# Optimization experiments

Hardware: AMD Instinct MI355X
Metric: run time of the kernel (lower is better)

The kernel has to match this reference:

```python
import jax, jax.numpy as jnp
import numpy as np

K = 3          # kernel_size
PAD = 1        # padding
FOCAL = 50.0
DMIN = 1.0
DMAX = 50.0
ORIG_H = 512.0  # original_image_size[1]


def setup_inputs() -> dict:
    key = jax.random.key(0)
    k1, k2 = jax.random.split(key)
    x = jax.random.normal(k1, (4, 64, 256, 256), dtype=jnp.float32)
    # conv weight [out_ch, in_ch, K, K] (bias=False)
    W = jax.random.normal(k2, (64, 64, K, K), dtype=jnp.float32) * 0.05
    return {"x": x, "W": W}


def _bilinear(img, xs, ys):
    """Bilinear sample img [B,C,H,W] at float pixel coords xs, ys [B,Ho,Wo].
    Zero padding outside the image (grid_sample semantics)."""
    B, C, H, Wd = img.shape
    Ho, Wo = xs.shape[1], xs.shape[2]
    x0 = jnp.floor(xs); y0 = jnp.floor(ys)
    wx1 = xs - x0; wx0 = 1.0 - wx1
    wy1 = ys - y0; wy0 = 1.0 - wy1
    img_flat = img.reshape(B, C, H * Wd)

    def gat(ix, iy):
        ixi = ix.astype(jnp.int32); iyi = iy.astype(jnp.int32)
        valid = (ixi >= 0) & (ixi < Wd) & (iyi >= 0) & (iyi < H)
        idx = jnp.clip(iyi, 0, H - 1) * Wd + jnp.clip(ixi, 0, Wd - 1)
        v = jnp.take_along_axis(img_flat, idx.reshape(B, 1, Ho * Wo), axis=2)
        v = v.reshape(B, C, Ho, Wo)
        return v * valid[:, None].astype(img.dtype)

    return (gat(x0, y0) * (wx0 * wy0)[:, None]
            + gat(x0 + 1, y0) * (wx1 * wy0)[:, None]
            + gat(x0, y0 + 1) * (wx0 * wy1)[:, None]
            + gat(x0 + 1, y0 + 1) * (wx1 * wy1)[:, None])


def reference(x, W):
    B, C, H, Wd = x.shape
    downsample = ORIG_H / H  # 2.0 for H=256

    # upper branch: plain 3x3 conv, padding 1, no bias
    x_upper = jax.lax.conv_general_dilated(x, W, (1, 1), [(PAD, PAD), (PAD, PAD)])

    # geometry -> clamped depth (geometry_method='max', formulation='depth')
    depth = jnp.clip(jnp.max(x, axis=1), DMIN, DMAX)  # [B,H,W]

    # Frontal homography: Hom01 = I with [1,2] = focal/(downsample*depth);
    # its inverse Hom10 shifts y by -s.
    s = FOCAL / (downsample * depth)  # [B,H,W]

    xi = jnp.arange(Wd, dtype=x.dtype)[None, None, :]
    yi = jnp.arange(H, dtype=x.dtype)[None, :, None]
    xs = jnp.broadcast_to(xi, (B, H, Wd))
    ys = yi - s  # Hom10 applied to pixel coords

    # warp input with per-pixel Hom10 (pass_warped_images=True)
    x2 = _bilinear(x, xs, ys)

    # deformable conv: per-pixel offset from Hom10 is (dx,dy)=(0,-s) for all 9 taps
    x_lower = jnp.zeros_like(x_upper)
    for ky in range(K):
        for kx in range(K):
            sx = xs + (kx - PAD)
            sy = ys + (ky - PAD)
            tap = _bilinear(x2, sx, sy)  # [B,C,H,W]
            x_lower = x_lower + jnp.einsum('bchw,oc->bohw', tap, W[:, :, ky, kx])

    # project with 'min' over the stacked (upper, lower) branches
    return jnp.minimum(x_upper, x_lower)
```

## Files before the change

### kernel.cpp

```cpp
#include <hip/hip_runtime.h>
#include <cmath>

constexpr int BB = 4, CC = 64, HH = 256, WW = 256;
constexpr int WP = 258;
constexpr int C2R = 257;

typedef short short8 __attribute__((ext_vector_type(8)));
typedef float f32x4 __attribute__((ext_vector_type(4)));
#define MFMA_BF16 __builtin_amdgcn_mfma_f32_16x16x32_bf16

union U16x8 { uint4 v; unsigned short h[8]; };

__device__ inline unsigned short f2bf(float f) {
  unsigned u = __builtin_bit_cast(unsigned, f);
  u += 0x7fffu + ((u >> 16) & 1u);
  return (unsigned short)(u >> 16);
}
__device__ inline float bf2f(unsigned short h) {
  unsigned u = ((unsigned)h) << 16;
  return __builtin_bit_cast(float, u);
}

__global__ __launch_bounds__(256, 2) void k_pack(const float* __restrict__ x,
                                                 float* __restrict__ s,
                                                 unsigned short* __restrict__ xn) {
  __shared__ float tile[CC * 257];
  const int t = threadIdx.x, y = blockIdx.x, b = blockIdx.y;
  const float* base = x + (size_t)b * CC * HH * WW + y * WW + t;
  float m = -1e30f;
#pragma unroll 8
  for (int c = 0; c < CC; ++c) {
    float v = base[(size_t)c * HH * WW];
    tile[c * 257 + t] = v;
    m = fmaxf(m, v);
  }
  s[(b * HH + y) * WW + t] = 25.0f / fminf(fmaxf(m, 1.0f), 50.0f);
  uint4* xn4 = (uint4*)xn;
  if (t < 16) {
    int col = (t >> 3) ? (WP - 1) : 0, c8 = t & 7;
    xn4[(((size_t)(b * HH + y) * WP + col) * CC + c8 * 8) >> 3] =
        make_uint4(0, 0, 0, 0);
  }
  __syncthreads();
#pragma unroll
  for (int g = 0; g < 8; ++g) {
    int px = g * 32 + (t >> 3), c8 = t & 7;
    U16x8 r;
#pragma unroll
    for (int j = 0; j < 8; ++j) r.h[j] = f2bf(tile[(c8 * 8 + j) * 257 + px]);
    xn4[(((size_t)(b * HH + y) * WP + px + 1) * CC + c8 * 8) >> 3] = r.v;
  }
}

__global__ __launch_bounds__(256) void k_wpack(const float* __restrict__ Wt,
                                               unsigned short* __restrict__ Wp) {
  int gid = blockIdx.x * 256 + threadIdx.x;
  int lane = gid & 63, kc = (gid >> 6) & 1, mt = (gid >> 7) & 3, tap = gid >> 9;
  int o = mt * 16 + (lane & 15);
  int kb = kc * 32 + (lane >> 4) * 8;
  int ky = tap / 3, kx = tap % 3;
  U16x8 r;
#pragma unroll
  for (int j = 0; j < 8; ++j)
    r.h[j] = f2bf(Wt[o * 576 + (kb + j) * 9 + ky * 3 + kx]);
  ((uint4*)Wp)[gid] = r.v;
}

__global__ __launch_bounds__(256) void k_warp(const unsigned short* __restrict__ xn,
                                              const float* __restrict__ s,
                                              unsigned short* __restrict__ x2) {
  const int t = threadIdx.x, r = blockIdx.x, b = blockIdx.y;
  const uint4* xn4 = (const uint4*)xn;
  uint4* x24 = (uint4*)x2;
  if (t < 16) {
    int col = (t >> 3) ? (WP - 1) : 0, c8 = t & 7;
    x24[(((size_t)(b * HH + r) * WP + col) * CC + c8 * 8) >> 3] =
        make_uint4(0, 0, 0, 0);
  }
#pragma unroll
  for (int g = 0; g < 8; ++g) {
    int px = g * 32 + (t >> 3), c8 = t & 7;
    float sv = s[(b * HH + r) * WW + px];
    float ys = (float)r - sv;
    float fy = floorf(ys);
    float wfr = ys - fy;
    int i0 = (int)fy;
    float w0 = (i0 >= 0 && i0 < HH) ? 1.0f - wfr : 0.0f;
    float w1 = (i0 + 1 >= 0 && i0 + 1 < HH) ? wfr : 0.0f;
    int a0 = min(max(i0, 0), HH - 1), a1 = min(max(i0 + 1, 0), HH - 1);
    U16x8 u0, u1, rr;
    u0.v = xn4[(((size_t)(b * HH + a0) * WP + px + 1) * CC + c8 * 8) >> 3];
    u1.v = xn4[(((size_t)(b * HH + a1) * WP + px + 1) * CC + c8 * 8) >> 3];
#pragma unroll
    for (int k = 0; k < 8; ++k)
      rr.h[k] = f2bf(w0 * bf2f(u0.h[k]) + w1 * bf2f(u1.h[k]));
    x24[(((size_t)(b * HH + r) * WP + px + 1) * CC + c8 * 8) >> 3] = rr.v;
  }
}

#define STAGE_TILE(src4, rowBase, colBase, bb)                                 \
  do {                                                                         \
    for (int i = 0; i < 13; ++i) {                                             \
      int idx = i * 256 + t;                                                   \
      if (idx < 3168) {                                                        \
        int rr_ = idx / 528, rem = idx % 528;                                  \
        int col_ = rem >> 3, ch_ = rem & 7;                                    \
        int xrow = (rowBase) + rr_;                                            \
        uint4 v = make_uint4(0, 0, 0, 0);                                      \
        if (xrow >= 0 && xrow < HH)                                            \
          v = src4[((size_t)((bb)*HH + xrow) * WP + (colBase) + col_) * 8 + ch_]; \
        lds[(rr_ * 66 + col_) * 8 + (ch_ ^ (col_ & 7))] = v;                   \
      }                                                                        \
    }                                                                          \
  } while (0)

__global__ __launch_bounds__(256, 2) void k_lower(const unsigned short* __restrict__ x2,
                                                  const unsigned short* __restrict__ Wp,
                                                  unsigned short* __restrict__ c2) {
  __shared__ uint4 lds[3168];
  const int t = threadIdx.x;
  const int ctile = blockIdx.x & 3, tr = blockIdx.x >> 2;
  const int b = blockIdx.y;
  const int r0 = tr * 4 - 1;
  const int colBase = ctile * 64;

  const uint4* src4 = (const uint4*)x2;
  STAGE_TILE(src4, r0 - 1, colBase, b);

  const int lane = t & 63, w = t >> 6;
  const int ow = w & 1, rg = w >> 1, lr = rg * 2;
  const int quad = lane >> 4, l15 = lane & 15;

  short8 wf[9][2][2];
  const uint4* wp4 = (const uint4*)Wp;
#pragma unroll
  for (int tap = 0; tap < 9; ++tap)
#pragma unroll
    for (int ct = 0; ct < 2; ++ct)
#pragma unroll
      for (int kc = 0; kc < 2; ++kc)
        wf[tap][ct][kc] = __builtin_bit_cast(
            short8, wp4[((tap * 4 + (ow * 2 + ct)) * 2 + kc) * 64 + lane]);
  __syncthreads();

#pragma unroll 1
  for (int pt = 0; pt < 4; ++pt) {
    f32x4 acc[2][2] = {{{0.f, 0.f, 0.f, 0.f}, {0.f, 0.f, 0.f, 0.f}},
                       {{0.f, 0.f, 0.f, 0.f}, {0.f, 0.f, 0.f, 0.f}}};
#pragma unroll
    for (int ir = 0; ir < 4; ++ir) {
      int ldr = lr + ir;
#pragma unroll
      for (int kx = 0; kx < 3; ++kx) {
        int col = pt * 16 + l15 + kx;
        int cb = (ldr * 66 + col) * 8, sw = col & 7;
#pragma unroll
        for (int kc = 0; kc < 2; ++kc) {
          short8 xf = __builtin_bit_cast(short8, lds[cb + ((kc * 4 + quad) ^ sw)]);
          if (ir <= 2) {
#pragma unroll
            for (int ct = 0; ct < 2; ++ct)
              acc[0][ct] = MFMA_BF16(wf[ir * 3 + kx][ct][kc], xf, acc[0][ct], 0, 0, 0);
          }
          if (ir >= 1) {
#pragma unroll
            for (int ct = 0; ct < 2; ++ct)
              acc[1][ct] = MFMA_BF16(wf[(ir - 1) * 3 + kx][ct][kc], xf, acc[1][ct], 0, 0, 0);
          }
        }
      }
    }
#pragma unroll
    for (int rr = 0; rr < 2; ++rr) {
      int r = r0 + lr + rr;
      if (r > 255) continue;
      int px = colBase + pt * 16 + l15;
#pragma unroll
      for (int ct = 0; ct < 2; ++ct) {
        f32x4 A = acc[rr][ct];
        int ch = (ow * 2 + ct) * 16 + quad * 4;
        unsigned short h0 = f2bf(A[0]), h1 = f2bf(A[1]), h2 = f2bf(A[2]), h3 = f2bf(A[3]);
        uint2 val = make_uint2((unsigned)h0 | ((unsigned)h1 << 16),
                               (unsigned)h2 | ((unsigned)h3 << 16));
        *(uint2*)(c2 + (((size_t)(b * C2R + (r + 1)) * WW + px) * CC + ch)) = val;
      }
    }
  }
}

__global__ __launch_bounds__(256, 2) void k_final(const unsigned short* __restrict__ xn,
                                                  const unsigned short* __restrict__ Wp,
                                                  const float* __restrict__ s,
                                                  const unsigned short* __restrict__ c2,
                                                  float* __restrict__ out) {
  __shared__ uint4 lds[3168];
  const int t = threadIdx.x;
  const int ctile = blockIdx.x & 3, tr = blockIdx.x >> 2;
  const int b = blockIdx.y;
  const int y0 = tr * 4;
  const int colBase = ctile * 64;

  const uint4* src4 = (const uint4*)xn;
  STAGE_TILE(src4, y0 - 1, colBase, b);

  const int lane = t & 63, w = t >> 6;
  const int ow = w & 1, rg = w >> 1, lr = rg * 2;
  const int quad = lane >> 4, l15 = lane & 15;

  short8 wf[9][2][2];
  const uint4* wp4 = (const uint4*)Wp;
#pragma unroll
  for (int tap = 0; tap < 9; ++tap)
#pragma unroll
    for (int ct = 0; ct < 2; ++ct)
#pragma unroll
      for (int kc = 0; kc < 2; ++kc)
        wf[tap][ct][kc] = __builtin_bit_cast(
            short8, wp4[((tap * 4 + (ow * 2 + ct)) * 2 + kc) * 64 + lane]);
  __syncthreads();

#pragma unroll 1
  for (int pt = 0; pt < 4; ++pt) {
    f32x4 acc[2][2] = {{{0.f, 0.f, 0.f, 0.f}, {0.f, 0.f, 0.f, 0.f}},
                       {{0.f, 0.f, 0.f, 0.f}, {0.f, 0.f, 0.f, 0.f}}};
#pragma unroll
    for (int ir = 0; ir < 4; ++ir) {
      int ldr = lr + ir;
#pragma unroll
      for (int kx = 0; kx < 3; ++kx) {
        int col = pt * 16 + l15 + kx;
        int cb = (ldr * 66 + col) * 8, sw = col & 7;
#pragma unroll
        for (int kc = 0; kc < 2; ++kc) {
          short8 xf = __builtin_bit_cast(short8, lds[cb + ((kc * 4 + quad) ^ sw)]);
          if (ir <= 2) {
#pragma unroll
            for (int ct = 0; ct < 2; ++ct)
              acc[0][ct] = MFMA_BF16(xf, wf[ir * 3 + kx][ct][kc], acc[0][ct], 0, 0, 0);
          }
          if (ir >= 1) {
#pragma unroll
            for (int ct = 0; ct < 2; ++ct)
              acc[1][ct] = MFMA_BF16(xf, wf[(ir - 1) * 3 + kx][ct][kc], acc[1][ct], 0, 0, 0);
          }
        }
      }
    }
#pragma unroll
    for (int rr = 0; rr < 2; ++rr) {
      int y = y0 + lr + rr;
      int px0 = colBase + pt * 16 + quad * 4;
      f32x4 sv4 = *(const f32x4*)(s + (b * HH + y) * WW + px0);
      float lw0[4], lw1[4];
      int a0i[4], a1i[4];
#pragma unroll
      for (int j = 0; j < 4; ++j) {
        float ys = (float)y - sv4[j];
        float fy = floorf(ys);
        float wfr = ys - fy;
        int i0 = (int)fy;
        lw0[j] = (i0 + 1 >= 0 && i0 + 1 <= HH) ? 1.0f - wfr : 0.0f;
        lw1[j] = (i0 + 2 >= 0 && i0 + 2 <= HH) ? wfr : 0.0f;
        a0i[j] = min(max(i0 + 1, 0), HH);
        a1i[j] = min(max(i0 + 2, 0), HH);
      }
#pragma unroll
      for (int ct = 0; ct < 2; ++ct) {
        f32x4 A = acc[rr][ct];
        int ch = (ow * 2 + ct) * 16 + l15;
        f32x4 res;
#pragma unroll
        for (int j = 0; j < 4; ++j) {
          int px = px0 + j;
          float v0 = bf2f(c2[((size_t)(b * C2R + a0i[j]) * WW + px) * CC + ch]);
          float v1 = bf2f(c2[((size_t)(b * C2R + a1i[j]) * WW + px) * CC + ch]);
          res[j] = fminf(A[j], lw0[j] * v0 + lw1[j] * v1);
        }
        *(f32x4*)(out + ((size_t)(b * CC + ch) * HH + y) * WW + px0) = res;
      }
    }
  }
}

extern "C" void kernel_launch(void* const* d_in, const int* in_sizes, int n_in,
                              void* d_out, int out_size, void* d_ws, size_t ws_size,
                              hipStream_t stream) {
  const float* x = (const float*)d_in[0];
  const float* Wt = (const float*)d_in[1];
  float* out = (float*)d_out;

  char* ws = (char*)d_ws;
  float* s = (float*)ws;
  unsigned short* Wp = (unsigned short*)(ws + 1048576);
  unsigned short* xn = (unsigned short*)(ws + 1122304);
  unsigned short* x2 = (unsigned short*)(ws + 34938880);
  unsigned short* c2 = (unsigned short*)(ws + 68755456);
  k_pack<<<dim3(HH, BB), 256, 0, stream>>>(x, s, xn);
  k_wpack<<<dim3(18), 256, 0, stream>>>(Wt, Wp);
  k_warp<<<dim3(HH, BB), 256, 0, stream>>>(xn, s, x2);
  k_lower<<<dim3(4 * 65, BB), 256, 0, stream>>>(x2, Wp, c2);
  k_final<<<dim3(4 * 64, BB), 256, 0, stream>>>(xn, Wp, s, c2, out);
}
```

Before: 216.6 us.

## Fuse vertical warp into lower-conv tile staging and transpose final MFMA output mapping

Removes the separate k_warp kernel and its x2 intermediate buffer, and recomputes the bilinear vertical warp on the fly while staging the input tile into LDS in k_lower. This cuts one launch and a full write plus read of a bf16 tensor, at the cost of recomputing the warp for halo rows and doing two gathered loads per staged element. The final kernel's MFMA operands are swapped so each lane holds four consecutive channels, which allows vectorized loads from c2 but turns the output stores into scalar strided writes. The fused path also rounds to bf16 by truncation instead of round-to-nearest.

```diff
diff --git a/kernel.cpp b/kernel.cpp
--- a/kernel.cpp
+++ b/kernel.cpp
@@ -10,11 +10,15 @@
 #define MFMA_BF16 __builtin_amdgcn_mfma_f32_16x16x32_bf16
 
 union U16x8 { uint4 v; unsigned short h[8]; };
+union U16x4 { uint2 v; unsigned short h[4]; };
 
 __device__ inline unsigned short f2bf(float f) {
   unsigned u = __builtin_bit_cast(unsigned, f);
   u += 0x7fffu + ((u >> 16) & 1u);
   return (unsigned short)(u >> 16);
+}
+__device__ inline unsigned short f2bf_trunc(float f) {
+  return (unsigned short)(__builtin_bit_cast(unsigned, f) >> 16);
 }
 __device__ inline float bf2f(unsigned short h) {
   unsigned u = ((unsigned)h) << 16;
@@ -64,38 +68,6 @@
   for (int j = 0; j < 8; ++j)
     r.h[j] = f2bf(Wt[o * 576 + (kb + j) * 9 + ky * 3 + kx]);
   ((uint4*)Wp)[gid] = r.v;
-}
-
-__global__ __launch_bounds__(256) void k_warp(const unsigned short* __restrict__ xn,
-                                              const float* __restrict__ s,
-                                              unsigned short* __restrict__ x2) {
-  const int t = threadIdx.x, r = blockIdx.x, b = blockIdx.y;
-  const uint4* xn4 = (const uint4*)xn;
-  uint4* x24 = (uint4*)x2;
-  if (t < 16) {
-    int col = (t >> 3) ? (WP - 1) : 0, c8 = t & 7;
-    x24[(((size_t)(b * HH + r) * WP + col) * CC + c8 * 8) >> 3] =
-        make_uint4(0, 0, 0, 0);
-  }
-#pragma unroll
-  for (int g = 0; g < 8; ++g) {
-    int px = g * 32 + (t >> 3), c8 = t & 7;
-    float sv = s[(b * HH + r) * WW + px];
-    float ys = (float)r - sv;
-    float fy = floorf(ys);
-    float wfr = ys - fy;
-    int i0 = (int)fy;
-    float w0 = (i0 >= 0 && i0 < HH) ? 1.0f - wfr : 0.0f;
-    float w1 = (i0 + 1 >= 0 && i0 + 1 < HH) ? wfr : 0.0f;
-    int a0 = min(max(i0, 0), HH - 1), a1 = min(max(i0 + 1, 0), HH - 1);
-    U16x8 u0, u1, rr;
-    u0.v = xn4[(((size_t)(b * HH + a0) * WP + px + 1) * CC + c8 * 8) >> 3];
-    u1.v = xn4[(((size_t)(b * HH + a1) * WP + px + 1) * CC + c8 * 8) >> 3];
-#pragma unroll
-    for (int k = 0; k < 8; ++k)
-      rr.h[k] = f2bf(w0 * bf2f(u0.h[k]) + w1 * bf2f(u1.h[k]));
-    x24[(((size_t)(b * HH + r) * WP + px + 1) * CC + c8 * 8) >> 3] = rr.v;
-  }
 }
 
 #define STAGE_TILE(src4, rowBase, colBase, bb)                                 \
@@ -114,8 +86,9 @@
     }                                                                          \
   } while (0)
 
-__global__ __launch_bounds__(256, 2) void k_lower(const unsigned short* __restrict__ x2,
+__global__ __launch_bounds__(256, 2) void k_lower(const unsigned short* __restrict__ xn,
                                                   const unsigned short* __restrict__ Wp,
+                                                  const float* __restrict__ s,
                                                   unsigned short* __restrict__ c2) {
   __shared__ uint4 lds[3168];
   const int t = threadIdx.x;
@@ -124,8 +97,36 @@
   const int r0 = tr * 4 - 1;
   const int colBase = ctile * 64;
 
-  const uint4* src4 = (const uint4*)x2;
-  STAGE_TILE(src4, r0 - 1, colBase, b);
+  const uint4* xn4 = (const uint4*)xn;
+  for (int i = 0; i < 13; ++i) {
+    int idx = i * 256 + t;
+    if (idx < 3168) {
+      int rr_ = idx / 528, rem = idx % 528;
+      int col_ = rem >> 3, ch_ = rem & 7;
+      int xrow = r0 - 1 + rr_;
+      uint4 v = make_uint4(0, 0, 0, 0);
+      if (xrow >= 0 && xrow < HH) {
+        int px = colBase + col_ - 1;
+        int pxc = min(max(px, 0), WW - 1);
+        float sv = s[(b * HH + xrow) * WW + pxc];
+        float ys = (float)xrow - sv;
+        float fy = floorf(ys);
+        float wfr = ys - fy;
+        int i0 = (int)fy;
+        float w0 = (i0 >= 0) ? 1.0f - wfr : 0.0f;
+        float w1 = (i0 + 1 >= 0) ? wfr : 0.0f;
+        int a0 = max(i0, 0), a1 = max(i0 + 1, 0);
+        U16x8 u0, u1, rr;
+        u0.v = xn4[((size_t)(b * HH + a0) * WP + colBase + col_) * 8 + ch_];
+        u1.v = xn4[((size_t)(b * HH + a1) * WP + colBase + col_) * 8 + ch_];
+#pragma unroll
+        for (int k = 0; k < 8; ++k)
+          rr.h[k] = f2bf_trunc(w0 * bf2f(u0.h[k]) + w1 * bf2f(u1.h[k]));
+        v = rr.v;
+      }
+      lds[(rr_ * 66 + col_) * 8 + (ch_ ^ (col_ & 7))] = v;
+    }
+  }
 
   const int lane = t & 63, w = t >> 6;
   const int ow = w & 1, rg = w >> 1, lr = rg * 2;
@@ -236,47 +237,42 @@
           if (ir <= 2) {
 #pragma unroll
             for (int ct = 0; ct < 2; ++ct)
-              acc[0][ct] = MFMA_BF16(xf, wf[ir * 3 + kx][ct][kc], acc[0][ct], 0, 0, 0);
+              acc[0][ct] = MFMA_BF16(wf[ir * 3 + kx][ct][kc], xf, acc[0][ct], 0, 0, 0);
           }
           if (ir >= 1) {
 #pragma unroll
             for (int ct = 0; ct < 2; ++ct)
-              acc[1][ct] = MFMA_BF16(xf, wf[(ir - 1) * 3 + kx][ct][kc], acc[1][ct], 0, 0, 0);
+              acc[1][ct] = MFMA_BF16(wf[(ir - 1) * 3 + kx][ct][kc], xf, acc[1][ct], 0, 0, 0);
           }
         }
       }
     }
+    int px = colBase + pt * 16 + l15;
 #pragma unroll
     for (int rr = 0; rr < 2; ++rr) {
       int y = y0 + lr + rr;
-      int px0 = colBase + pt * 16 + quad * 4;
-      f32x4 sv4 = *(const f32x4*)(s + (b * HH + y) * WW + px0);
-      float lw0[4], lw1[4];
-      int a0i[4], a1i[4];
-#pragma unroll
-      for (int j = 0; j < 4; ++j) {
-        float ys = (float)y - sv4[j];
-        float fy = floorf(ys);
-        float wfr = ys - fy;
-        int i0 = (int)fy;
-        lw0[j] = (i0 + 1 >= 0 && i0 + 1 <= HH) ? 1.0f - wfr : 0.0f;
-        lw1[j] = (i0 + 2 >= 0 && i0 + 2 <= HH) ? wfr : 0.0f;
-        a0i[j] = min(max(i0 + 1, 0), HH);
-        a1i[j] = min(max(i0 + 2, 0), HH);
-      }
+      float sv = s[(b * HH + y) * WW + px];
+      float ys = (float)y - sv;
+      float fy = floorf(ys);
+      float wfr = ys - fy;
+      int i0 = (int)fy;
+      float lw0 = (i0 + 1 >= 0 && i0 + 1 <= HH) ? 1.0f - wfr : 0.0f;
+      float lw1 = (i0 + 2 >= 0 && i0 + 2 <= HH) ? wfr : 0.0f;
+      int a0 = min(max(i0 + 1, 0), HH);
+      int a1 = min(max(i0 + 2, 0), HH);
 #pragma unroll
       for (int ct = 0; ct < 2; ++ct) {
         f32x4 A = acc[rr][ct];
-        int ch = (ow * 2 + ct) * 16 + l15;
-        f32x4 res;
-#pragma unroll
-        for (int j = 0; j < 4; ++j) {
-          int px = px0 + j;
-          float v0 = bf2f(c2[((size_t)(b * C2R + a0i[j]) * WW + px) * CC + ch]);
-          float v1 = bf2f(c2[((size_t)(b * C2R + a1i[j]) * WW + px) * CC + ch]);
-          res[j] = fminf(A[j], lw0[j] * v0 + lw1[j] * v1);
+        int ch = (ow * 2 + ct) * 16 + quad * 4;
+        U16x4 v0, v1;
+        v0.v = *(const uint2*)(c2 + ((size_t)(b * C2R + a0) * WW + px) * CC + ch);
+        v1.v = *(const uint2*)(c2 + ((size_t)(b * C2R + a1) * WW + px) * CC + ch);
+#pragma unroll
+        for (int reg = 0; reg < 4; ++reg) {
+          float lower = lw0 * bf2f(v0.h[reg]) + lw1 * bf2f(v1.h[reg]);
+          out[((size_t)(b * CC + ch + reg) * HH + y) * WW + px] =
+              fminf(A[reg], lower);
         }
-        *(f32x4*)(out + ((size_t)(b * CC + ch) * HH + y) * WW + px0) = res;
       }
     }
   }
@@ -293,11 +289,9 @@
   float* s = (float*)ws;
   unsigned short* Wp = (unsigned short*)(ws + 1048576);
   unsigned short* xn = (unsigned short*)(ws + 1122304);
-  unsigned short* x2 = (unsigned short*)(ws + 34938880);
-  unsigned short* c2 = (unsigned short*)(ws + 68755456);
+  unsigned short* c2 = (unsigned short*)(ws + 34938880);
   k_pack<<<dim3(HH, BB), 256, 0, stream>>>(x, s, xn);
   k_wpack<<<dim3(18), 256, 0, stream>>>(Wt, Wp);
-  k_warp<<<dim3(HH, BB), 256, 0, stream>>>(xn, s, x2);
-  k_lower<<<dim3(4 * 65, BB), 256, 0, stream>>>(x2, Wp, c2);
+  k_lower<<<dim3(4 * 65, BB), 256, 0, stream>>>(xn, Wp, s, c2);
   k_final<<<dim3(4 * 64, BB), 256, 0, stream>>>(xn, Wp, s, c2, out);
 }
```

After: 197.2 us. -8.9%, faster.
